# Kernel tuning notes

Measured on AMD Instinct MI355X. Metric: run time of the kernel, lower is better.

## Reference

```python
import jax, jax.numpy as jnp
import numpy as np

N_SERIES = 1024
N_TIME = 600
INPUT_SIZE = 168
OUTPUT_SIZE = 24
N_S = 4
SEAS = 24  # single seasonality period


def setup_inputs() -> dict:
    key = jax.random.key(0)
    k1, k2, k3 = jax.random.split(key, 3)
    # strictly positive series (Holt-Winters multiplicative form divides and logs)
    y = jax.random.uniform(k1, (N_SERIES, N_TIME), jnp.float32) + 0.5
    s_matrix = jax.random.normal(k2, (N_SERIES, N_S), jnp.float32)
    embeds = jax.random.uniform(k3, (N_SERIES, 1 + 1 + SEAS), jnp.float32)
    idxs = jnp.arange(N_SERIES, dtype=jnp.int32)
    return {"y": y, "s_matrix": s_matrix, "embeds": embeds, "idxs": idxs}


def _compute_levels_seasons(y, embeds_rows):
    # embeds_rows: (N, 26) = [lev_sms_logit, seas_sms_logit, 24 log init seasons]
    lev_sms = jax.nn.sigmoid(embeds_rows[:, 0])           # (N,)
    seas_sms = jax.nn.sigmoid(embeds_rows[:, 1])          # (N,)
    init_seas = jnp.exp(embeds_rows[:, 2:2 + SEAS])       # (N, P)

    level0 = y[:, 0] / init_seas[:, 0]                    # (N,)
    # buffer holds seasonalities1[t .. t+P-1]; before step t=1 that is
    # [init[1], ..., init[P-1], init[0]]
    buf0 = jnp.roll(init_seas, -1, axis=1)                # (N, P)

    def step(carry, y_t):
        lev_prev, buf = carry
        s_t = buf[:, 0]
        newlev = lev_sms * (y_t / s_t) + (1.0 - lev_sms) * lev_prev
        news = seas_sms * (y_t / newlev) + (1.0 - seas_sms) * s_t
        buf = jnp.concatenate([buf[:, 1:], news[:, None]], axis=1)
        return (newlev, buf), (newlev, news)

    (_, _), (levs, seas_new) = jax.lax.scan(step, (level0, buf0), y[:, 1:].T)
    levels = jnp.concatenate([level0[:, None], levs.T], axis=1)          # (N, T)
    # seasonalities1 indices 0..P are [init[0..P-1], init[0]], then one new per step
    seas_head = jnp.concatenate([init_seas, init_seas[:, :1]], axis=1)   # (N, P+1)
    seasonalities1 = jnp.concatenate([seas_head, seas_new.T], axis=1)    # (N, T+P)
    return levels, seasonalities1


def reference(y, s_matrix, embeds, idxs):
    embeds_rows = embeds[idxs]                                 # (N, 26)
    levels, seasonalities1 = _compute_levels_seasons(y, embeds_rows)

    n_series, n_time = y.shape
    n_windows = n_time - INPUT_SIZE - OUTPUT_SIZE + 1          # 409
    w = jnp.arange(n_windows)
    idx_in = w[:, None] + jnp.arange(INPUT_SIZE)               # (W, I)
    idx_out = w[:, None] + INPUT_SIZE + jnp.arange(OUTPUT_SIZE)  # (W, O)

    y_in = y[:, idx_in]                                        # (N, W, I)
    lev_end = levels[:, w + INPUT_SIZE - 1]                    # (N, W)
    seas_in = seasonalities1[:, idx_in]                        # (N, W, I)
    y_in_norm = jnp.log(y_in / (lev_end[:, :, None] * seas_in))
    insample = jnp.transpose(y_in_norm, (1, 0, 2))             # (W, N, I)
    static = jnp.broadcast_to(s_matrix[None], (n_windows, n_series, s_matrix.shape[1]))
    windows_y_insample = jnp.concatenate([insample, static], axis=2)  # (W, N, I+n_s)

    # eval mode: outsample windows are raw (un-normalized) targets
    windows_y_outsample = jnp.transpose(y[:, idx_out], (1, 0, 2))     # (W, N, O)

    return (windows_y_insample, windows_y_outsample, levels, seasonalities1)
```

## Files before the change

### kernel.cpp

```cpp
#include <hip/hip_runtime.h>

#define N_SERIES 1024
#define N_TIME 600
#define INPUT_SIZE 168
#define OUTPUT_SIZE 24
#define N_S 4
#define SEAS 24
#define N_WINDOWS (N_TIME - INPUT_SIZE - OUTPUT_SIZE + 1)
#define SEAS_LEN (N_TIME + SEAS)

#define INS_ELEMS (N_WINDOWS * N_SERIES * (INPUT_SIZE + N_S))
#define OUTS_ELEMS (N_WINDOWS * N_SERIES * OUTPUT_SIZE)
#define LEV_ELEMS (N_SERIES * N_TIME)
#define SEAS_ELEMS (N_SERIES * SEAS_LEN)

#define NQ_OUTS (OUTS_ELEMS / 4)

#define SCAN_BLOCKS 16
#define SCAN_T 64
#define COPY_BLOCKS 2032

#define INS3_BLOCKS 256
#define INS3_T 512
#define TASKS_PER_W 172
#define TASKS_TOTAL (N_WINDOWS * TASKS_PER_W)

typedef float f4 __attribute__((ext_vector_type(4)));

#define WAVE_FENCE()                                   \
    do {                                               \
        __builtin_amdgcn_wave_barrier();               \
        asm volatile("" ::: "memory");                 \
    } while (0)

__global__ __launch_bounds__(SCAN_T) void scan_copy_kernel(
    const float* __restrict__ y, const float* __restrict__ embeds,
    const int* __restrict__ idxs, float* __restrict__ levels,
    float* __restrict__ seas1, f4* __restrict__ out_outs)
{
    __shared__ float b_lev[SCAN_T][25];
    __shared__ float b_sea[SCAN_T][25];

    if (blockIdx.x < SCAN_BLOCKS) {
        const int lane = threadIdx.x;
        const int s0 = blockIdx.x * SCAN_T;
        const int s = s0 + lane;
        const int row = idxs[s];
        const float* e = embeds + row * (2 + SEAS);

        const float lev_sms = 1.0f / (1.0f + __expf(-e[0]));
        const float seas_sms = 1.0f / (1.0f + __expf(-e[1]));
        const float one_m_lev = 1.0f - lev_sms;
        const float one_m_seas = 1.0f - seas_sms;

        const float* yrow = y + s * N_TIME;
        const f4* yv4 = (const f4*)yrow;

        f4 cur[6], nxt[6];
#pragma unroll
        for (int i = 0; i < 6; ++i) cur[i] = yv4[i];

        float sb[SEAS];
#pragma unroll
        for (int j = 0; j < SEAS; ++j) {
            float v = __expf(e[2 + j]);
            sb[j] = v;
            b_sea[lane][j] = v;
        }
        WAVE_FENCE();
#pragma unroll
        for (int k4 = 0; k4 < 6; ++k4) {
            int q4 = lane + k4 * SCAN_T;
            int r = q4 / 6;
            int c4 = q4 - r * 6;
            int cc = c4 * 4;
            f4 v = {b_sea[r][cc], b_sea[r][cc + 1], b_sea[r][cc + 2],
                    b_sea[r][cc + 3]};
            *(f4*)(seas1 + (s0 + r) * SEAS_LEN + cc) = v;
        }
        seas1[s * SEAS_LEN + SEAS] = sb[0];
        float lev = __fdividef(cur[0].x, sb[0]);
        levels[s * N_TIME] = lev;
        WAVE_FENCE();

        {
#pragma unroll
            for (int i = 0; i < 6; ++i) nxt[i] = yv4[6 + i];
#pragma unroll
            for (int j = 0; j < 23; ++j) {
                const int t = j + 1;
                float yt = cur[t >> 2][t & 3];
                float st = sb[t];
                float q1 = __fdividef(yt, st);
                float newlev = lev_sms * q1 + one_m_lev * lev;
                float news =
                    seas_sms * __fdividef(yt, newlev) + one_m_seas * st;
                lev = newlev;
                sb[t] = news;
                b_lev[lane][j] = newlev;
                b_sea[lane][j] = news;
            }
            WAVE_FENCE();
#pragma unroll
            for (int k = 0; k < 24; ++k) {
                int i = lane + k * SCAN_T;
                int r = i / 24;
                int col = i - r * 24;
                if (col < 23) {
                    int sr = s0 + r;
                    levels[sr * N_TIME + 1 + col] = b_lev[r][col];
                    seas1[sr * SEAS_LEN + 25 + col] = b_sea[r][col];
                }
            }
            WAVE_FENCE();
#pragma unroll
            for (int i = 0; i < 6; ++i) cur[i] = nxt[i];
        }

#pragma unroll 1
        for (int c = 1; c < 25; ++c) {
            const int t0 = 24 * c;
            if (c < 24) {
                const f4* p = (const f4*)(yrow + 24 * (c + 1));
#pragma unroll
                for (int i = 0; i < 6; ++i) nxt[i] = p[i];
            }
#pragma unroll
            for (int j = 0; j < 24; ++j) {
                float yt = cur[j >> 2][j & 3];
                float st = sb[j];
                float q1 = __fdividef(yt, st);
                float newlev = lev_sms * q1 + one_m_lev * lev;
                float news =
                    seas_sms * __fdividef(yt, newlev) + one_m_seas * st;
                lev = newlev;
                sb[j] = news;
                b_lev[lane][j] = newlev;
                b_sea[lane][j] = news;
            }
            WAVE_FENCE();
#pragma unroll
            for (int k4 = 0; k4 < 6; ++k4) {
                int q4 = lane + k4 * SCAN_T;
                int r = q4 / 6;
                int c4 = q4 - r * 6;
                int sr = s0 + r;
                int cc = c4 * 4;
                f4 vl = {b_lev[r][cc], b_lev[r][cc + 1], b_lev[r][cc + 2],
                         b_lev[r][cc + 3]};
                *(f4*)(levels + sr * N_TIME + t0 + cc) = vl;
                f4 vs = {b_sea[r][cc], b_sea[r][cc + 1], b_sea[r][cc + 2],
                         b_sea[r][cc + 3]};
                *(f4*)(seas1 + sr * SEAS_LEN + SEAS + t0 + cc) = vs;
            }
            WAVE_FENCE();
#pragma unroll
            for (int i = 0; i < 6; ++i) cur[i] = nxt[i];
        }
    } else {
        int idx = (blockIdx.x - SCAN_BLOCKS) * SCAN_T + threadIdx.x;
        const int stride = (gridDim.x - SCAN_BLOCKS) * SCAN_T;
        for (; idx < NQ_OUTS; idx += stride) {
            int rowq = idx / 6;
            int j4 = idx - rowq * 6;
            int w = rowq >> 10;
            int s = rowq & 1023;
            const float* yp = y + s * N_TIME + w + INPUT_SIZE + j4 * 4;
            f4 v = {yp[0], yp[1], yp[2], yp[3]};
            __builtin_nontemporal_store(v, &out_outs[idx]);
        }
    }
}

__global__ __launch_bounds__(INS3_T) void ins3_kernel(
    const float* __restrict__ y, const float* __restrict__ levels,
    const float* __restrict__ seas1, const float* __restrict__ s_matrix,
    f4* __restrict__ out_ins)
{
    __shared__ float tq[4][4][152];
    __shared__ float lv[4][608];
    __shared__ f4 sml[4];

    const int tid = threadIdx.x;
    const int s0 = blockIdx.x * 4;

    for (int i = tid; i < 600; i += INS3_T) {
        int sl = i / 150;
        int c = i - sl * 150;
        int s = s0 + sl;
        f4 yv = *((const f4*)(y + s * N_TIME) + c);
        f4 sv = *((const f4*)(seas1 + s * SEAS_LEN) + c);
        f4 lvv = *((const f4*)(levels + s * N_TIME) + c);
        tq[sl][0][c] = __logf(__fdividef(yv.x, sv.x));
        tq[sl][1][c] = __logf(__fdividef(yv.y, sv.y));
        tq[sl][2][c] = __logf(__fdividef(yv.z, sv.z));
        tq[sl][3][c] = __logf(__fdividef(yv.w, sv.w));
        f4 lg = {__logf(lvv.x), __logf(lvv.y), __logf(lvv.z), __logf(lvv.w)};
        *(f4*)(&lv[sl][4 * c]) = lg;
    }
    if (tid < 4) sml[tid] = *((const f4*)s_matrix + (s0 + tid));
    __syncthreads();

    for (int ql = tid; ql < TASKS_TOTAL; ql += INS3_T) {
        unsigned uql = (unsigned)ql;
        int w = uql / 172u;
        int slot = ql - w * 172;
        int sl = (unsigned)slot / 43u;
        int e4 = slot - sl * 43;
        f4 v;
        if (e4 == 42) {
            v = sml[sl];
        } else {
            float l = lv[sl][w + INPUT_SIZE - 1];
            int a0 = w, a1 = w + 1, a2 = w + 2, a3 = w + 3;
            v.x = tq[sl][a0 & 3][(a0 >> 2) + e4] - l;
            v.y = tq[sl][a1 & 3][(a1 >> 2) + e4] - l;
            v.z = tq[sl][a2 & 3][(a2 >> 2) + e4] - l;
            v.w = tq[sl][a3 & 3][(a3 >> 2) + e4] - l;
        }
        __builtin_nontemporal_store(
            v, &out_ins[w * (N_SERIES * 43) + (s0 + sl) * 43 + e4]);
    }
}

extern "C" void kernel_launch(void* const* d_in, const int* in_sizes, int n_in,
                              void* d_out, int out_size, void* d_ws, size_t ws_size,
                              hipStream_t stream) {
    const float* y      = (const float*)d_in[0];
    const float* sm     = (const float*)d_in[1];
    const float* embeds = (const float*)d_in[2];
    const int*   idxs   = (const int*)d_in[3];

    float* out      = (float*)d_out;
    float* out_ins  = out;
    float* out_outs = out + INS_ELEMS;
    float* out_lev  = out + INS_ELEMS + OUTS_ELEMS;
    float* out_seas = out_lev + LEV_ELEMS;

    (void)d_ws; (void)ws_size;

    scan_copy_kernel<<<SCAN_BLOCKS + COPY_BLOCKS, SCAN_T, 0, stream>>>(
        y, embeds, idxs, out_lev, out_seas, (f4*)out_outs);
    ins3_kernel<<<INS3_BLOCKS, INS3_T, 0, stream>>>(
        y, out_lev, out_seas, sm, (f4*)out_ins);
}
```

Measured before the change: 112.5 us.

## Split insample kernel across window segments and drop LDS staging in scan

The insample-writing kernel now launches 2048 blocks of 256 threads instead of 256 blocks of 512. Each block covers four series and a 52-window segment, so it precomputes only 224 timesteps of log-ratio and log-level data instead of the full rows. This is meant to raise occupancy and spread the dominant output-store traffic over more waves, at the cost of recomputing overlapping log values across segments. The scan path also drops its shared-memory transpose and wave fences and writes levels and seasonalities straight from per-thread f4 registers. That cuts LDS traffic and sync, but each lane now writes its own strided row instead of the wave producing coalesced stores.

```diff
diff --git a/kernel.cpp b/kernel.cpp
--- a/kernel.cpp
+++ b/kernel.cpp
@@ -12,7 +12,6 @@
 #define INS_ELEMS (N_WINDOWS * N_SERIES * (INPUT_SIZE + N_S))
 #define OUTS_ELEMS (N_WINDOWS * N_SERIES * OUTPUT_SIZE)
 #define LEV_ELEMS (N_SERIES * N_TIME)
-#define SEAS_ELEMS (N_SERIES * SEAS_LEN)
 
 #define NQ_OUTS (OUTS_ELEMS / 4)
 
@@ -20,31 +19,19 @@
 #define SCAN_T 64
 #define COPY_BLOCKS 2032
 
-#define INS3_BLOCKS 256
-#define INS3_T 512
-#define TASKS_PER_W 172
-#define TASKS_TOTAL (N_WINDOWS * TASKS_PER_W)
+#define INS4_BLOCKS 2048
+#define WSEG 52
 
 typedef float f4 __attribute__((ext_vector_type(4)));
-
-#define WAVE_FENCE()                                   \
-    do {                                               \
-        __builtin_amdgcn_wave_barrier();               \
-        asm volatile("" ::: "memory");                 \
-    } while (0)
 
 __global__ __launch_bounds__(SCAN_T) void scan_copy_kernel(
     const float* __restrict__ y, const float* __restrict__ embeds,
     const int* __restrict__ idxs, float* __restrict__ levels,
     float* __restrict__ seas1, f4* __restrict__ out_outs)
 {
-    __shared__ float b_lev[SCAN_T][25];
-    __shared__ float b_sea[SCAN_T][25];
-
     if (blockIdx.x < SCAN_BLOCKS) {
         const int lane = threadIdx.x;
-        const int s0 = blockIdx.x * SCAN_T;
-        const int s = s0 + lane;
+        const int s = blockIdx.x * SCAN_T + lane;
         const int row = idxs[s];
         const float* e = embeds + row * (2 + SEAS);
 
@@ -55,6 +42,8 @@
 
         const float* yrow = y + s * N_TIME;
         const f4* yv4 = (const f4*)yrow;
+        float* lrow = levels + s * N_TIME;
+        float* srow = seas1 + s * SEAS_LEN;
 
         f4 cur[6], nxt[6];
 #pragma unroll
@@ -62,57 +51,40 @@
 
         float sb[SEAS];
 #pragma unroll
-        for (int j = 0; j < SEAS; ++j) {
-            float v = __expf(e[2 + j]);
-            sb[j] = v;
-            b_sea[lane][j] = v;
-        }
-        WAVE_FENCE();
-#pragma unroll
-        for (int k4 = 0; k4 < 6; ++k4) {
-            int q4 = lane + k4 * SCAN_T;
-            int r = q4 / 6;
-            int c4 = q4 - r * 6;
-            int cc = c4 * 4;
-            f4 v = {b_sea[r][cc], b_sea[r][cc + 1], b_sea[r][cc + 2],
-                    b_sea[r][cc + 3]};
-            *(f4*)(seas1 + (s0 + r) * SEAS_LEN + cc) = v;
-        }
-        seas1[s * SEAS_LEN + SEAS] = sb[0];
+        for (int j = 0; j < SEAS; ++j) sb[j] = __expf(e[2 + j]);
+
+#pragma unroll
+        for (int k = 0; k < 6; ++k) {
+            f4 v = {sb[4 * k], sb[4 * k + 1], sb[4 * k + 2], sb[4 * k + 3]};
+            *(f4*)(srow + 4 * k) = v;
+        }
+
         float lev = __fdividef(cur[0].x, sb[0]);
-        levels[s * N_TIME] = lev;
-        WAVE_FENCE();
-
+
+        f4 fl[6], fs[6];
+        fl[0].x = lev;
+        fs[0].x = sb[0];
         {
 #pragma unroll
             for (int i = 0; i < 6; ++i) nxt[i] = yv4[6 + i];
 #pragma unroll
-            for (int j = 0; j < 23; ++j) {
-                const int t = j + 1;
-                float yt = cur[t >> 2][t & 3];
-                float st = sb[t];
+            for (int j = 1; j < 24; ++j) {
+                float yt = cur[j >> 2][j & 3];
+                float st = sb[j];
                 float q1 = __fdividef(yt, st);
                 float newlev = lev_sms * q1 + one_m_lev * lev;
                 float news =
                     seas_sms * __fdividef(yt, newlev) + one_m_seas * st;
                 lev = newlev;
-                sb[t] = news;
-                b_lev[lane][j] = newlev;
-                b_sea[lane][j] = news;
-            }
-            WAVE_FENCE();
-#pragma unroll
-            for (int k = 0; k < 24; ++k) {
-                int i = lane + k * SCAN_T;
-                int r = i / 24;
-                int col = i - r * 24;
-                if (col < 23) {
-                    int sr = s0 + r;
-                    levels[sr * N_TIME + 1 + col] = b_lev[r][col];
-                    seas1[sr * SEAS_LEN + 25 + col] = b_sea[r][col];
-                }
-            }
-            WAVE_FENCE();
+                sb[j] = news;
+                fl[j >> 2][j & 3] = newlev;
+                fs[j >> 2][j & 3] = news;
+            }
+#pragma unroll
+            for (int k = 0; k < 6; ++k) {
+                *(f4*)(lrow + 4 * k) = fl[k];
+                *(f4*)(srow + SEAS + 4 * k) = fs[k];
+            }
 #pragma unroll
             for (int i = 0; i < 6; ++i) cur[i] = nxt[i];
         }
@@ -135,25 +107,14 @@
                     seas_sms * __fdividef(yt, newlev) + one_m_seas * st;
                 lev = newlev;
                 sb[j] = news;
-                b_lev[lane][j] = newlev;
-                b_sea[lane][j] = news;
-            }
-            WAVE_FENCE();
-#pragma unroll
-            for (int k4 = 0; k4 < 6; ++k4) {
-                int q4 = lane + k4 * SCAN_T;
-                int r = q4 / 6;
-                int c4 = q4 - r * 6;
-                int sr = s0 + r;
-                int cc = c4 * 4;
-                f4 vl = {b_lev[r][cc], b_lev[r][cc + 1], b_lev[r][cc + 2],
-                         b_lev[r][cc + 3]};
-                *(f4*)(levels + sr * N_TIME + t0 + cc) = vl;
-                f4 vs = {b_sea[r][cc], b_sea[r][cc + 1], b_sea[r][cc + 2],
-                         b_sea[r][cc + 3]};
-                *(f4*)(seas1 + sr * SEAS_LEN + SEAS + t0 + cc) = vs;
-            }
-            WAVE_FENCE();
+                fl[j >> 2][j & 3] = newlev;
+                fs[j >> 2][j & 3] = news;
+            }
+#pragma unroll
+            for (int k = 0; k < 6; ++k) {
+                *(f4*)(lrow + t0 + 4 * k) = fl[k];
+                *(f4*)(srow + SEAS + t0 + 4 * k) = fs[k];
+            }
 #pragma unroll
             for (int i = 0; i < 6; ++i) cur[i] = nxt[i];
         }
@@ -172,54 +133,60 @@
     }
 }
 
-__global__ __launch_bounds__(INS3_T) void ins3_kernel(
+__global__ __launch_bounds__(256) void ins4_kernel(
     const float* __restrict__ y, const float* __restrict__ levels,
     const float* __restrict__ seas1, const float* __restrict__ s_matrix,
     f4* __restrict__ out_ins)
 {
-    __shared__ float tq[4][4][152];
-    __shared__ float lv[4][608];
+    __shared__ __align__(16) float tq[4][4][57];
+    __shared__ __align__(16) float llv[4][224];
     __shared__ f4 sml[4];
 
     const int tid = threadIdx.x;
-    const int s0 = blockIdx.x * 4;
-
-    for (int i = tid; i < 600; i += INS3_T) {
-        int sl = i / 150;
-        int c = i - sl * 150;
+    const int g = blockIdx.x >> 3;
+    const int seg = blockIdx.x & 7;
+    const int s0 = g * 4;
+    const int w0 = seg * WSEG;
+    const int nw = (seg == 7) ? (N_WINDOWS - 7 * WSEG) : WSEG;
+
+    for (int i = tid; i < 224; i += 256) {
+        int sl = i / 56;
+        int c = i - sl * 56;
         int s = s0 + sl;
-        f4 yv = *((const f4*)(y + s * N_TIME) + c);
-        f4 sv = *((const f4*)(seas1 + s * SEAS_LEN) + c);
-        f4 lvv = *((const f4*)(levels + s * N_TIME) + c);
+        int t = w0 + 4 * c;
+        f4 yv = *(const f4*)(y + s * N_TIME + t);
+        f4 sv = *(const f4*)(seas1 + s * SEAS_LEN + t);
+        f4 lv = *(const f4*)(levels + s * N_TIME + t);
         tq[sl][0][c] = __logf(__fdividef(yv.x, sv.x));
         tq[sl][1][c] = __logf(__fdividef(yv.y, sv.y));
         tq[sl][2][c] = __logf(__fdividef(yv.z, sv.z));
         tq[sl][3][c] = __logf(__fdividef(yv.w, sv.w));
-        f4 lg = {__logf(lvv.x), __logf(lvv.y), __logf(lvv.z), __logf(lvv.w)};
-        *(f4*)(&lv[sl][4 * c]) = lg;
+        f4 lg = {__logf(lv.x), __logf(lv.y), __logf(lv.z), __logf(lv.w)};
+        *(f4*)(&llv[sl][4 * c]) = lg;
     }
     if (tid < 4) sml[tid] = *((const f4*)s_matrix + (s0 + tid));
     __syncthreads();
 
-    for (int ql = tid; ql < TASKS_TOTAL; ql += INS3_T) {
-        unsigned uql = (unsigned)ql;
-        int w = uql / 172u;
-        int slot = ql - w * 172;
-        int sl = (unsigned)slot / 43u;
-        int e4 = slot - sl * 43;
+    const int ntask = nw * 172;
+    for (int ql = tid; ql < ntask; ql += 256) {
+        int wp = ql / 172;
+        int slot = ql - 172 * wp;
+        int sl = slot / 43;
+        int e4 = slot - 43 * sl;
         f4 v;
         if (e4 == 42) {
             v = sml[sl];
         } else {
-            float l = lv[sl][w + INPUT_SIZE - 1];
-            int a0 = w, a1 = w + 1, a2 = w + 2, a3 = w + 3;
+            float l = llv[sl][wp + 167];
+            int a0 = wp, a1 = wp + 1, a2 = wp + 2, a3 = wp + 3;
             v.x = tq[sl][a0 & 3][(a0 >> 2) + e4] - l;
             v.y = tq[sl][a1 & 3][(a1 >> 2) + e4] - l;
             v.z = tq[sl][a2 & 3][(a2 >> 2) + e4] - l;
             v.w = tq[sl][a3 & 3][(a3 >> 2) + e4] - l;
         }
         __builtin_nontemporal_store(
-            v, &out_ins[w * (N_SERIES * 43) + (s0 + sl) * 43 + e4]);
+            v,
+            (f4*)out_ins + ((w0 + wp) * (N_SERIES * 43) + (s0 + sl) * 43 + e4));
     }
 }
 
@@ -241,6 +208,6 @@
 
     scan_copy_kernel<<<SCAN_BLOCKS + COPY_BLOCKS, SCAN_T, 0, stream>>>(
         y, embeds, idxs, out_lev, out_seas, (f4*)out_outs);
-    ins3_kernel<<<INS3_BLOCKS, INS3_T, 0, stream>>>(
+    ins4_kernel<<<INS4_BLOCKS, 256, 0, stream>>>(
         y, out_lev, out_seas, sm, (f4*)out_ins);
 }
```

Result: faster. 108.9 us (median of 2 runs) (-3.2%).
